# Performance work log

Hardware: AMD Instinct MI355X
Metric: run time of the kernel (lower is better)

The kernel has to match this reference:

```python
import jax, jax.numpy as jnp
import numpy as np
from jax import lax

NUM_LAYERS = 128
SEQ_LEN = 256
H = 1  # hidden_size = input_size = 1


def setup_inputs() -> dict:
    key = jax.random.key(0)
    k = jax.random.split(key, 5)
    # PyTorch GRU init: U(-1/sqrt(H), 1/sqrt(H)) with H=1 -> U(-1, 1)
    u = lambda kk, shp: jax.random.uniform(kk, shp, jnp.float32, -1.0, 1.0)
    return {
        "x": jax.random.normal(k[0], (1, SEQ_LEN), jnp.float32),
        "w_ih": u(k[1], (NUM_LAYERS, 3 * H, H)),  # gates stacked [r, z, n]
        "w_hh": u(k[2], (NUM_LAYERS, 3 * H, H)),
        "b_ih": u(k[3], (NUM_LAYERS, 3 * H)),
        "b_hh": u(k[4], (NUM_LAYERS, 3 * H)),
    }


def _gru_stack(x_seq, w_ih, w_hh, b_ih, b_hh):
    # x_seq: [T, H]; params stacked over layers. PyTorch GRU equations, gate order r,z,n.
    def layer_step(seq, params):
        wi, wh, bi, bh = params  # [3H,H], [3H,H], [3H], [3H]

        def cell(h, xt):  # h: [H], xt: [H]
            gi = wi @ xt + bi  # [3H]
            gh = wh @ h + bh   # [3H]
            r = jax.nn.sigmoid(gi[0:H] + gh[0:H])
            z = jax.nn.sigmoid(gi[H:2 * H] + gh[H:2 * H])
            n = jnp.tanh(gi[2 * H:] + r * gh[2 * H:])
            h_new = (1.0 - z) * n + z * h
            return h_new, h_new

        h0 = jnp.zeros((H,), dtype=seq.dtype)
        _, out = lax.scan(cell, h0, seq)  # out: [T, H]
        return out, None

    out, _ = lax.scan(layer_step, x_seq, (w_ih, w_hh, b_ih, b_hh))
    return out


def reference(x, w_ih, w_hh, b_ih, b_hh):
    # x: [1, T] -> GRU input [T, H=1] (unbatched), encoder only (decoder unused in forward)
    seq = x.T  # [T, 1]
    out = _gru_stack(seq, w_ih, w_hh, b_ih, b_hh)  # [T, 1]
    return out.T  # [1, T]
```

## Files before the change

kernel.cpp:

```cpp
#include <hip/hip_runtime.h>

#define T_LEN 256
#define N_LAYERS 128

__device__ __forceinline__ float ex2(float x) { return __builtin_amdgcn_exp2f(x); }
__device__ __forceinline__ float rcp1p(float e) { return __builtin_amdgcn_rcpf(1.0f + e); }

__device__ __forceinline__ float dpp_wave_shr1(float v) {
    int i = __float_as_int(v);
    int r = __builtin_amdgcn_update_dpp(i, i, 0x138, 0xF, 0xF, false);
    return __int_as_float(r);
}

__global__ __launch_bounds__(64, 1) void gru_stack_wavefront(
    const float* __restrict__ x,
    const float* __restrict__ w_ih,
    const float* __restrict__ w_hh,
    const float* __restrict__ b_ih,
    const float* __restrict__ b_hh,
    float* __restrict__ out)
{
    __shared__ float sx[T_LEN];
    const int lane = threadIdx.x;

    #pragma unroll
    for (int i = 0; i < T_LEN / 64; ++i)
        sx[lane + 64 * i] = x[lane + 64 * i];

    const int la = 2 * lane, lb = 2 * lane + 1;
    const float L1 = -1.4426950408889634f;
    const float L2 = -2.8853900817779268f;

    const float wiAr = L1 * w_ih[3 * la + 0], whAr = L1 * w_hh[3 * la + 0];
    const float bAr  = L1 * (b_ih[3 * la + 0] + b_hh[3 * la + 0]);
    const float wiAz = L1 * w_ih[3 * la + 1], whAz = L1 * w_hh[3 * la + 1];
    const float bAz  = L1 * (b_ih[3 * la + 1] + b_hh[3 * la + 1]);
    const float wiAn = L2 * w_ih[3 * la + 2], biAn = L2 * b_ih[3 * la + 2];
    const float whAn = L2 * w_hh[3 * la + 2], bhAn = L2 * b_hh[3 * la + 2];
    const float wiBr = L1 * w_ih[3 * lb + 0], whBr = L1 * w_hh[3 * lb + 0];
    const float bBr  = L1 * (b_ih[3 * lb + 0] + b_hh[3 * lb + 0]);
    const float wiBz = L1 * w_ih[3 * lb + 1], whBz = L1 * w_hh[3 * lb + 1];
    const float bBz  = L1 * (b_ih[3 * lb + 1] + b_hh[3 * lb + 1]);
    const float wiBn = L2 * w_ih[3 * lb + 2], biBn = L2 * b_ih[3 * lb + 2];
    const float whBn = L2 * w_hh[3 * lb + 2], bhBn = L2 * b_hh[3 * lb + 2];

    float hA = 0.0f, hB = 0.0f;
    float cAr = bAr, cAz = bAz, gAn = bhAn;
    float cBr = bBr, cBz = bBz, gBn = bhBn;

    __syncthreads();

    float out_val = 0.0f;
    float xcur = sx[0];
    const bool is_l0 = (lane == 0);
    const bool is_l63 = (lane == 63);

    #pragma unroll 4
    for (int s = 0; s < T_LEN + 63; ++s) {
        float shifted = dpp_wave_shr1(out_val);
        float in = is_l0 ? xcur : shifted;
        float xnext = sx[(s + 1) & (T_LEN - 1)];

        const int t = s - lane;
        const bool valid = (unsigned)t < (unsigned)T_LEN;

        float rA = rcp1p(ex2(fmaf(wiAr, in, cAr)));
        float zA = rcp1p(ex2(fmaf(wiAz, in, cAz)));
        float nA = fmaf(2.0f, rcp1p(ex2(fmaf(rA, gAn, fmaf(wiAn, in, biAn)))), -1.0f);
        float hAn = fmaf(zA, hA - nA, nA);
        hA = valid ? hAn : hA;
        cAr = fmaf(whAr, hA, bAr);
        cAz = fmaf(whAz, hA, bAz);
        gAn = fmaf(whAn, hA, bhAn);

        float rB = rcp1p(ex2(fmaf(wiBr, hA, cBr)));
        float zB = rcp1p(ex2(fmaf(wiBz, hA, cBz)));
        float nB = fmaf(2.0f, rcp1p(ex2(fmaf(rB, gBn, fmaf(wiBn, hA, biBn)))), -1.0f);
        float hBn = fmaf(zB, hB - nB, nB);
        hB = valid ? hBn : hB;
        cBr = fmaf(whBr, hB, bBr);
        cBz = fmaf(whBz, hB, bBz);
        gBn = fmaf(whBn, hB, bhBn);

        out_val = hB;
        if (is_l63 && valid) out[t] = hB;

        xcur = xnext;
    }
}

extern "C" void kernel_launch(void* const* d_in, const int* in_sizes, int n_in,
                              void* d_out, int out_size, void* d_ws, size_t ws_size,
                              hipStream_t stream) {
    const float* x    = (const float*)d_in[0];
    const float* w_ih = (const float*)d_in[1];
    const float* w_hh = (const float*)d_in[2];
    const float* b_ih = (const float*)d_in[3];
    const float* b_hh = (const float*)d_in[4];
    float* out = (float*)d_out;

    gru_stack_wavefront<<<1, 64, 0, stream>>>(x, w_ih, w_hh, b_ih, b_hh, out);
}
```

Baseline: 100.5 us.

## Skew the two per-lane GRU layers so they run in parallel with packed FMAs

Each lane still owns two layers, but the second layer now consumes the first layer's output from the previous step instead of the current one. That makes the two cell updates in a step independent, so they can be expressed as 2-wide vectors with packed FMA. It also removes the shared-memory staging of x: inputs are held in registers and fed to lane 0 by rotating them across the wave with DPP. The goal is to halve the serial dependency chain per step, at the cost of a deeper pipeline (384 steps instead of 319).

```diff
diff --git a/kernel.cpp b/kernel.cpp
--- a/kernel.cpp
+++ b/kernel.cpp
@@ -3,13 +3,19 @@
 #define T_LEN 256
 #define N_LAYERS 128
 
+typedef float f2 __attribute__((ext_vector_type(2)));
+
 __device__ __forceinline__ float ex2(float x) { return __builtin_amdgcn_exp2f(x); }
-__device__ __forceinline__ float rcp1p(float e) { return __builtin_amdgcn_rcpf(1.0f + e); }
+__device__ __forceinline__ float rcpf_(float x) { return __builtin_amdgcn_rcpf(x); }
+__device__ __forceinline__ f2 pk_fma(f2 a, f2 b, f2 c) { return __builtin_elementwise_fma(a, b, c); }
 
 __device__ __forceinline__ float dpp_wave_shr1(float v) {
     int i = __float_as_int(v);
-    int r = __builtin_amdgcn_update_dpp(i, i, 0x138, 0xF, 0xF, false);
-    return __int_as_float(r);
+    return __int_as_float(__builtin_amdgcn_update_dpp(i, i, 0x138, 0xF, 0xF, false));
+}
+__device__ __forceinline__ float dpp_wave_rol1(float v) {
+    int i = __float_as_int(v);
+    return __int_as_float(__builtin_amdgcn_update_dpp(i, i, 0x134, 0xF, 0xF, false));
 }
 
 __global__ __launch_bounds__(64, 1) void gru_stack_wavefront(
@@ -20,72 +26,83 @@
     const float* __restrict__ b_hh,
     float* __restrict__ out)
 {
-    __shared__ float sx[T_LEN];
     const int lane = threadIdx.x;
-
-    #pragma unroll
-    for (int i = 0; i < T_LEN / 64; ++i)
-        sx[lane + 64 * i] = x[lane + 64 * i];
-
     const int la = 2 * lane, lb = 2 * lane + 1;
     const float L1 = -1.4426950408889634f;
     const float L2 = -2.8853900817779268f;
 
-    const float wiAr = L1 * w_ih[3 * la + 0], whAr = L1 * w_hh[3 * la + 0];
-    const float bAr  = L1 * (b_ih[3 * la + 0] + b_hh[3 * la + 0]);
-    const float wiAz = L1 * w_ih[3 * la + 1], whAz = L1 * w_hh[3 * la + 1];
-    const float bAz  = L1 * (b_ih[3 * la + 1] + b_hh[3 * la + 1]);
-    const float wiAn = L2 * w_ih[3 * la + 2], biAn = L2 * b_ih[3 * la + 2];
-    const float whAn = L2 * w_hh[3 * la + 2], bhAn = L2 * b_hh[3 * la + 2];
-    const float wiBr = L1 * w_ih[3 * lb + 0], whBr = L1 * w_hh[3 * lb + 0];
-    const float bBr  = L1 * (b_ih[3 * lb + 0] + b_hh[3 * lb + 0]);
-    const float wiBz = L1 * w_ih[3 * lb + 1], whBz = L1 * w_hh[3 * lb + 1];
-    const float bBz  = L1 * (b_ih[3 * lb + 1] + b_hh[3 * lb + 1]);
-    const float wiBn = L2 * w_ih[3 * lb + 2], biBn = L2 * b_ih[3 * lb + 2];
-    const float whBn = L2 * w_hh[3 * lb + 2], bhBn = L2 * b_hh[3 * lb + 2];
+    f2 wi_r = { L1 * w_ih[3 * la + 0], L1 * w_ih[3 * lb + 0] };
+    f2 wi_z = { L1 * w_ih[3 * la + 1], L1 * w_ih[3 * lb + 1] };
+    f2 wi_n = { L2 * w_ih[3 * la + 2], L2 * w_ih[3 * lb + 2] };
+    f2 wh_r = { L1 * w_hh[3 * la + 0], L1 * w_hh[3 * lb + 0] };
+    f2 wh_z = { L1 * w_hh[3 * la + 1], L1 * w_hh[3 * lb + 1] };
+    f2 wh_n = { L2 * w_hh[3 * la + 2], L2 * w_hh[3 * lb + 2] };
+    f2 b_r  = { L1 * (b_ih[3 * la + 0] + b_hh[3 * la + 0]),
+                L1 * (b_ih[3 * lb + 0] + b_hh[3 * lb + 0]) };
+    f2 b_z  = { L1 * (b_ih[3 * la + 1] + b_hh[3 * la + 1]),
+                L1 * (b_ih[3 * lb + 1] + b_hh[3 * lb + 1]) };
+    f2 bi_n = { L2 * b_ih[3 * la + 2], L2 * b_ih[3 * lb + 2] };
+    f2 bh_n = { L2 * b_hh[3 * la + 2], L2 * b_hh[3 * lb + 2] };
 
-    float hA = 0.0f, hB = 0.0f;
-    float cAr = bAr, cAz = bAz, gAn = bhAn;
-    float cBr = bBr, cBz = bBz, gBn = bhBn;
+    float xc0 = x[lane];
+    float xc1 = x[lane + 64];
+    float xc2 = x[lane + 128];
+    float xc3 = x[lane + 192];
 
-    __syncthreads();
+    f2 h = { 0.0f, 0.0f };
+    f2 c_r = b_r, c_z = b_z, g_n = bh_n;
 
-    float out_val = 0.0f;
-    float xcur = sx[0];
+    const f2 one2 = { 1.0f, 1.0f };
+    const f2 two2 = { 2.0f, 2.0f };
+    const f2 mone2 = { -1.0f, -1.0f };
+
     const bool is_l0 = (lane == 0);
-    const bool is_l63 = (lane == 63);
+    int tA = -2 * lane - 1;
 
-    #pragma unroll 4
-    for (int s = 0; s < T_LEN + 63; ++s) {
-        float shifted = dpp_wave_shr1(out_val);
-        float in = is_l0 ? xcur : shifted;
-        float xnext = sx[(s + 1) & (T_LEN - 1)];
+    for (int blk = 0; blk < 6; ++blk) {
+        float xq;
+        if      (blk == 0) xq = xc0;
+        else if (blk == 1) xq = xc1;
+        else if (blk == 2) xq = xc2;
+        else               xq = xc3;
 
-        const int t = s - lane;
-        const bool valid = (unsigned)t < (unsigned)T_LEN;
+        #pragma unroll 8
+        for (int k = 0; k < 64; ++k) {
+            ++tA;
+            const bool validA = (unsigned)tA < (unsigned)T_LEN;
+            const bool validB = (unsigned)(tA - 1) < (unsigned)T_LEN;
 
-        float rA = rcp1p(ex2(fmaf(wiAr, in, cAr)));
-        float zA = rcp1p(ex2(fmaf(wiAz, in, cAz)));
-        float nA = fmaf(2.0f, rcp1p(ex2(fmaf(rA, gAn, fmaf(wiAn, in, biAn)))), -1.0f);
-        float hAn = fmaf(zA, hA - nA, nA);
-        hA = valid ? hAn : hA;
-        cAr = fmaf(whAr, hA, bAr);
-        cAz = fmaf(whAz, hA, bAz);
-        gAn = fmaf(whAn, hA, bhAn);
+            float shifted = dpp_wave_shr1(h.y);
+            float inA = is_l0 ? xq : shifted;
+            f2 in2 = { inA, h.x };
 
-        float rB = rcp1p(ex2(fmaf(wiBr, hA, cBr)));
-        float zB = rcp1p(ex2(fmaf(wiBz, hA, cBz)));
-        float nB = fmaf(2.0f, rcp1p(ex2(fmaf(rB, gBn, fmaf(wiBn, hA, biBn)))), -1.0f);
-        float hBn = fmaf(zB, hB - nB, nB);
-        hB = valid ? hBn : hB;
-        cBr = fmaf(whBr, hB, bBr);
-        cBz = fmaf(whBz, hB, bBz);
-        gBn = fmaf(whBn, hB, bhBn);
+            f2 u_r = pk_fma(wi_r, in2, c_r);
+            f2 u_z = pk_fma(wi_z, in2, c_z);
+            f2 u_n0 = pk_fma(wi_n, in2, bi_n);
+            f2 e_r = { ex2(u_r.x), ex2(u_r.y) };
+            f2 e_z = { ex2(u_z.x), ex2(u_z.y) };
+            f2 d_r = e_r + one2;
+            f2 d_z = e_z + one2;
+            f2 r2 = { rcpf_(d_r.x), rcpf_(d_r.y) };
+            f2 z2 = { rcpf_(d_z.x), rcpf_(d_z.y) };
+            f2 u_n = pk_fma(r2, g_n, u_n0);
+            f2 e_n = { ex2(u_n.x), ex2(u_n.y) };
+            f2 d_n = e_n + one2;
+            f2 s_n = { rcpf_(d_n.x), rcpf_(d_n.y) };
+            f2 n2 = pk_fma(two2, s_n, mone2);
+            f2 hn = pk_fma(z2, h - n2, n2);
 
-        out_val = hB;
-        if (is_l63 && valid) out[t] = hB;
+            h.x = validA ? hn.x : h.x;
+            h.y = validB ? hn.y : h.y;
 
-        xcur = xnext;
+            c_r = pk_fma(wh_r, h, b_r);
+            c_z = pk_fma(wh_z, h, b_z);
+            g_n = pk_fma(wh_n, h, bh_n);
+
+            if (lane == 63 && validB) out[tA - 1] = h.y;
+
+            xq = dpp_wave_rol1(xq);
+        }
     }
 }
 
```

Measured after the change: 108.3 us. +7.8%, slower.
